# Kernel tuning notes

Measured on AMD Instinct MI355X. Metric: run time of the kernel, lower is better.

The kernel has to match this reference:

```python
import jax, jax.numpy as jnp
import numpy as np

COMMITMENT_COST = 0.25
NUM_EMBEDDINGS = 1024
EMBEDDING_DIM = 256


def setup_inputs() -> dict:
    key = jax.random.key(0)
    k1, k2 = jax.random.split(key)
    inputs = jax.random.normal(k1, (64, 256, 32, 32), dtype=jnp.float32)
    emb_w = jax.random.normal(k2, (NUM_EMBEDDINGS, EMBEDDING_DIM), dtype=jnp.float32)
    return {"inputs": inputs, "emb_w": emb_w}


def reference(inputs, emb_w):
    # NCHW -> NHWC, flatten to [N, D]
    x = jnp.transpose(inputs, (0, 2, 3, 1))  # [B, H, W, D]
    B, H, W, D = x.shape
    flat = x.reshape(-1, D)  # [N, D]

    distances = (
        jnp.sum(flat * flat, axis=1, keepdims=True)
        + jnp.sum(emb_w * emb_w, axis=1)
        - 2.0 * flat @ emb_w.T
    )
    idx = jnp.argmin(distances, axis=1)  # [N]

    # one-hot @ W is just a gather of codebook rows
    quantized = emb_w[idx].reshape(B, H, W, D)

    # avg_probs = mean of one-hot encodings = normalized codeword counts
    counts = jnp.zeros((NUM_EMBEDDINGS,), dtype=jnp.float32).at[idx].add(1.0)
    avg_probs = counts / flat.shape[0]
    perplexity = jnp.exp(-jnp.sum(avg_probs * jnp.log(avg_probs + 1e-10)))

    e_latent_loss = jnp.mean((jax.lax.stop_gradient(quantized) - x) ** 2)
    loss = COMMITMENT_COST * e_latent_loss

    # straight-through estimator
    quantized_st = x + jax.lax.stop_gradient(quantized - x)
    quantized_out = jnp.transpose(quantized_st, (0, 3, 1, 2))  # back to NCHW

    return loss, quantized_out, perplexity, idx.reshape(B, H, W)
```

## Files before the change

### kernel.cpp

```cpp
#include <hip/hip_runtime.h>
#include <hip/hip_bf16.h>
#include <math.h>

typedef _Float16 f16;
typedef __attribute__((ext_vector_type(8))) _Float16 f16x8;
typedef __attribute__((ext_vector_type(16))) float f32x16;

#define DIMS 256
#define NCODE 1024
#define NPTS 65536

#define OUT_Q_OFF 1
#define OUT_PERP_OFF 16777217
#define OUT_IDX_OFF 16777218

#define EHI_F32_OFF 4
#define ELO_F32_OFF (4 + 131072)

#define ESTRIDE 264
#define XSTRIDE 132

__global__ __launch_bounds__(256) void k_eprep(const float* __restrict__ ew,
                                               f16* __restrict__ ehi,
                                               f16* __restrict__ elo,
                                               float* __restrict__ enorm) {
    int w = threadIdx.x >> 6;
    int l = threadIdx.x & 63;
    int row = blockIdx.x * 4 + w;
    float4 v = *reinterpret_cast<const float4*>(ew + (size_t)row * DIMS + l * 4);
    float vv[4] = {v.x, v.y, v.z, v.w};
    __align__(8) f16 hh[4];
    __align__(8) f16 ll[4];
    float s = 0.0f;
    #pragma unroll
    for (int e = 0; e < 4; ++e) {
        f16 h = (f16)vv[e];
        hh[e] = h;
        ll[e] = (f16)(vv[e] - (float)h);
        s += vv[e] * vv[e];
    }
    *reinterpret_cast<float2*>(ehi + (size_t)row * DIMS + l * 4) = *reinterpret_cast<float2*>(hh);
    *reinterpret_cast<float2*>(elo + (size_t)row * DIMS + l * 4) = *reinterpret_cast<float2*>(ll);
    #pragma unroll
    for (int off = 32; off > 0; off >>= 1) s += __shfl_down(s, off);
    if (l == 0) enorm[row] = s;
}

__global__ __launch_bounds__(256, 2) void k_argmin_mfma(const float* __restrict__ x,
                                                        const f16* __restrict__ ehi,
                                                        const f16* __restrict__ elo,
                                                        const float* __restrict__ enorm,
                                                        int* __restrict__ out_idx) {
    __shared__ __align__(16) char smem[2 * 32 * ESTRIDE * 2];
    __shared__ float enorm_lds[NCODE];
    float* Xs = (float*)smem;
    f16* EHI = (f16*)smem;
    f16* ELO = (f16*)(smem + 32 * ESTRIDE * 2);

    const int t = threadIdx.x;
    const int wave = t >> 6;
    const int lane = t & 63;
    const int lrow = lane & 31;
    const int lhalf = lane >> 5;

    const int blk = blockIdx.x;
    const int b = blk >> 3;
    const int hw0 = (blk & 7) << 7;
    const float* xb = x + (size_t)b * (DIMS * 1024) + hw0;

    #pragma unroll
    for (int i = 0; i < 4; ++i) enorm_lds[t + 256 * i] = enorm[t + 256 * i];

    f16x8 ahi[16], alo[16];
    #pragma unroll
    for (int dc = 0; dc < 4; ++dc) {
        __syncthreads();
        #pragma unroll
        for (int i = 0; i < 8; ++i) {
            int d = (t >> 5) + 8 * i;
            int p4 = (t & 31) * 4;
            float4 v = *reinterpret_cast<const float4*>(xb + (size_t)(dc * 64 + d) * 1024 + p4);
            *reinterpret_cast<float4*>(&Xs[d * XSTRIDE + p4]) = v;
        }
        __syncthreads();
        int p = wave * 32 + lrow;
        #pragma unroll
        for (int kcl = 0; kcl < 4; ++kcl) {
            f16x8 h, l;
            #pragma unroll
            for (int e = 0; e < 8; ++e) {
                float xv = Xs[(kcl * 16 + lhalf * 8 + e) * XSTRIDE + p];
                f16 hi = (f16)xv;
                h[e] = hi;
                l[e] = (f16)(xv - (float)hi);
            }
            ahi[dc * 4 + kcl] = h;
            alo[dc * 4 + kcl] = l;
        }
    }

    float bestv[16];
    int besti[16];
    #pragma unroll
    for (int r = 0; r < 16; ++r) { bestv[r] = 3.4e38f; besti[r] = 0; }

    for (int rd = 0; rd < 32; ++rd) {
        const int code0 = rd * 32;
        __syncthreads();
        #pragma unroll
        for (int j = 0; j < 4; ++j) {
            int q = t + 256 * j;
            int row = q >> 5;
            int cc = q & 31;
            const f16* sh = ehi + (size_t)(code0 + row) * DIMS + cc * 8;
            const f16* sl = elo + (size_t)(code0 + row) * DIMS + cc * 8;
            float4 vh = *reinterpret_cast<const float4*>(sh);
            float4 vl = *reinterpret_cast<const float4*>(sl);
            *reinterpret_cast<float4*>((char*)EHI + row * (ESTRIDE * 2) + cc * 16) = vh;
            *reinterpret_cast<float4*>((char*)ELO + row * (ESTRIDE * 2) + cc * 16) = vl;
        }
        __syncthreads();

        f32x16 acc;
        #pragma unroll
        for (int r = 0; r < 16; ++r) acc[r] = 0.0f;

        #pragma unroll
        for (int kc = 0; kc < 16; ++kc) {
            f16x8 bh = *reinterpret_cast<const f16x8*>(
                (const char*)EHI + lrow * (ESTRIDE * 2) + (kc * 2 + lhalf) * 16);
            f16x8 bl = *reinterpret_cast<const f16x8*>(
                (const char*)ELO + lrow * (ESTRIDE * 2) + (kc * 2 + lhalf) * 16);
            acc = __builtin_amdgcn_mfma_f32_32x32x16_f16(ahi[kc], bh, acc, 0, 0, 0);
            acc = __builtin_amdgcn_mfma_f32_32x32x16_f16(ahi[kc], bl, acc, 0, 0, 0);
            acc = __builtin_amdgcn_mfma_f32_32x32x16_f16(alo[kc], bh, acc, 0, 0, 0);
        }

        float en = enorm_lds[code0 + lrow];
        int cw = code0 + lrow;
        #pragma unroll
        for (int r = 0; r < 16; ++r) {
            float s = fmaf(-2.0f, acc[r], en);
            if (s < bestv[r]) { bestv[r] = s; besti[r] = cw; }
        }
    }

    #pragma unroll
    for (int off = 1; off <= 16; off <<= 1) {
        #pragma unroll
        for (int r = 0; r < 16; ++r) {
            float ov = __shfl_xor(bestv[r], off);
            int oi = __shfl_xor(besti[r], off);
            if (ov < bestv[r] || (ov == bestv[r] && oi < besti[r])) {
                bestv[r] = ov;
                besti[r] = oi;
            }
        }
    }
    if (lrow == 0) {
        #pragma unroll
        for (int r = 0; r < 16; ++r) {
            int row = (r & 3) + 8 * (r >> 2) + 4 * lhalf;
            out_idx[blk * 128 + wave * 32 + row] = besti[r];
        }
    }
}

#define QSTRIDE 258
__global__ __launch_bounds__(512) void k_quant(const float* __restrict__ x,
                                               const float* __restrict__ ew,
                                               const int* __restrict__ idxv,
                                               float* __restrict__ out,
                                               float* __restrict__ loss_acc) {
    __shared__ float Eq[64 * QSTRIDE];
    __shared__ int ids[64];
    const int t = threadIdx.x;
    const int blk = blockIdx.x;
    const int b = blk >> 4;
    const int hw0 = (blk & 15) << 6;

    if (t < 64) ids[t] = idxv[(b << 10) + hw0 + t];
    __syncthreads();

    #pragma unroll
    for (int i = 0; i < 8; ++i) {
        int f = i * 512 + t;
        int row = f >> 6;
        int c4 = f & 63;
        float4 v = *reinterpret_cast<const float4*>(ew + (size_t)ids[row] * DIMS + c4 * 4);
        float2 lo2 = {v.x, v.y};
        float2 hi2 = {v.z, v.w};
        *reinterpret_cast<float2*>(&Eq[row * QSTRIDE + c4 * 4]) = lo2;
        *reinterpret_cast<float2*>(&Eq[row * QSTRIDE + c4 * 4 + 2]) = hi2;
    }
    __syncthreads();

    const int p = t & 63;
    const int c0 = t >> 6;
    float lsum = 0.0f;
    #pragma unroll
    for (int k = 0; k < 32; ++k) {
        int c = k * 8 + c0;
        unsigned g = ((unsigned)b << 18) | ((unsigned)c << 10) | (unsigned)(hw0 + p);
        float xv = x[g];
        float q = Eq[p * QSTRIDE + c];
        float d = q - xv;
        out[OUT_Q_OFF + g] = xv + d;
        lsum += d * d;
    }
    #pragma unroll
    for (int off = 32; off > 0; off >>= 1) lsum += __shfl_down(lsum, off);
    if ((t & 63) == 0) atomicAdd(&loss_acc[blk & 63], lsum);
}

__global__ __launch_bounds__(256) void k_hist(const int* __restrict__ idxv,
                                              int* __restrict__ counts,
                                              float* __restrict__ out) {
    __shared__ int h[NCODE];
    int t = threadIdx.x;
    #pragma unroll
    for (int i = 0; i < 4; ++i) h[t + 256 * i] = 0;
    __syncthreads();
    int base = blockIdx.x * 1024;
    #pragma unroll
    for (int i = 0; i < 4; ++i) {
        int n = base + t + 256 * i;
        int id = idxv[n];
        out[OUT_IDX_OFF + n] = (float)id;
        atomicAdd(&h[id], 1);
    }
    __syncthreads();
    #pragma unroll
    for (int i = 0; i < 4; ++i) {
        int v = h[t + 256 * i];
        if (v) atomicAdd(&counts[t + 256 * i], v);
    }
}

__global__ __launch_bounds__(256) void k_final(const int* __restrict__ counts,
                                               const float* __restrict__ loss_acc,
                                               float* __restrict__ out) {
    int t = threadIdx.x;
    float s = 0.0f;
    #pragma unroll
    for (int i = 0; i < 4; ++i) {
        int cnt = counts[t + 256 * i];
        float p = (float)cnt * (1.0f / 65536.0f);
        s += p * logf(p + 1e-10f);
    }
    #pragma unroll
    for (int off = 32; off > 0; off >>= 1) s += __shfl_down(s, off);
    __shared__ float wsum[4];
    if ((t & 63) == 0) wsum[t >> 6] = s;
    __syncthreads();
    if (t == 0) {
        float S = wsum[0] + wsum[1] + wsum[2] + wsum[3];
        out[OUT_PERP_OFF] = expf(-S);
        float ls = 0.0f;
        for (int i = 0; i < 64; ++i) ls += loss_acc[i];
        out[0] = 0.25f * (ls * (1.0f / 16777216.0f));
    }
}

extern "C" void kernel_launch(void* const* d_in, const int* in_sizes, int n_in,
                              void* d_out, int out_size, void* d_ws, size_t ws_size,
                              hipStream_t stream) {
    const float* x = (const float*)d_in[0];
    const float* ew = (const float*)d_in[1];
    float* out = (float*)d_out;
    float* ws = (float*)d_ws;

    float* loss_acc = ws;
    int* counts = (int*)(ws + 64);
    float* enorm = ws + 64 + 1024;
    int* idxv = (int*)(ws + 64 + 2048);

    f16* ehi = (f16*)(out + EHI_F32_OFF);
    f16* elo = (f16*)(out + ELO_F32_OFF);

    hipMemsetAsync(d_ws, 0, (64 + 1024) * sizeof(float), stream);

    k_eprep<<<256, 256, 0, stream>>>(ew, ehi, elo, enorm);
    k_argmin_mfma<<<512, 256, 0, stream>>>(x, ehi, elo, enorm, idxv);
    k_quant<<<1024, 512, 0, stream>>>(x, ew, idxv, out, loss_acc);
    k_hist<<<64, 256, 0, stream>>>(idxv, counts, out);
    k_final<<<1, 256, 0, stream>>>(counts, loss_acc, out);
}
```

Measured before the change: 200.4 us.

## Double-buffer codebook tiles via direct global-to-LDS loads with XOR-swizzled layout

The codebook prep kernel now writes the hi/lo fp16 planes in a pre-tiled, XOR-swizzled 32-row tile layout. The argmin kernel streams each tile straight into LDS with global_load_lds, double-buffered so the next tile's load overlaps the current tile's MFMA work. This removes the register round-trip and one of the two barriers per round, and the swizzle replaces padding to avoid LDS bank conflicts. LDS use grows to 64KB plus the norms, which may limit how many blocks fit per CU.

```diff
diff --git a/kernel.cpp b/kernel.cpp
--- a/kernel.cpp
+++ b/kernel.cpp
@@ -16,13 +16,19 @@
 
 #define EHI_F32_OFF 4
 #define ELO_F32_OFF (4 + 131072)
-
-#define ESTRIDE 264
+#define TILE_BYTES 16384
+
 #define XSTRIDE 132
 
+__device__ __forceinline__ void gload_lds16(const void* g, void* l) {
+    __builtin_amdgcn_global_load_lds(
+        (const __attribute__((address_space(1))) unsigned int*)g,
+        (__attribute__((address_space(3))) unsigned int*)l, 16, 0, 0);
+}
+
 __global__ __launch_bounds__(256) void k_eprep(const float* __restrict__ ew,
-                                               f16* __restrict__ ehi,
-                                               f16* __restrict__ elo,
+                                               char* __restrict__ ehi,
+                                               char* __restrict__ elo,
                                                float* __restrict__ enorm) {
     int w = threadIdx.x >> 6;
     int l = threadIdx.x & 63;
@@ -39,23 +45,23 @@
         ll[e] = (f16)(vv[e] - (float)h);
         s += vv[e] * vv[e];
     }
-    *reinterpret_cast<float2*>(ehi + (size_t)row * DIMS + l * 4) = *reinterpret_cast<float2*>(hh);
-    *reinterpret_cast<float2*>(elo + (size_t)row * DIMS + l * 4) = *reinterpret_cast<float2*>(ll);
-    #pragma unroll
-    for (int off = 32; off > 0; off >>= 1) s += __shfl_down(s, off);
+    size_t off = (size_t)(row >> 5) * TILE_BYTES + (size_t)(row & 31) * 512
+               + (size_t)((((l >> 1) ^ (row & 7)) << 4) + ((l & 1) << 3));
+    *reinterpret_cast<float2*>(ehi + off) = *reinterpret_cast<float2*>(hh);
+    *reinterpret_cast<float2*>(elo + off) = *reinterpret_cast<float2*>(ll);
+    #pragma unroll
+    for (int off2 = 32; off2 > 0; off2 >>= 1) s += __shfl_down(s, off2);
     if (l == 0) enorm[row] = s;
 }
 
 __global__ __launch_bounds__(256, 2) void k_argmin_mfma(const float* __restrict__ x,
-                                                        const f16* __restrict__ ehi,
-                                                        const f16* __restrict__ elo,
+                                                        const char* __restrict__ ehi,
+                                                        const char* __restrict__ elo,
                                                         const float* __restrict__ enorm,
                                                         int* __restrict__ out_idx) {
-    __shared__ __align__(16) char smem[2 * 32 * ESTRIDE * 2];
+    __shared__ __align__(16) char smem[2 * 2 * TILE_BYTES];
     __shared__ float enorm_lds[NCODE];
     float* Xs = (float*)smem;
-    f16* EHI = (f16*)smem;
-    f16* ELO = (f16*)(smem + 32 * ESTRIDE * 2);
 
     const int t = threadIdx.x;
     const int wave = t >> 6;
@@ -98,44 +104,54 @@
             alo[dc * 4 + kcl] = l;
         }
     }
+    __syncthreads();
+
+    const char* gplane = (wave >> 1) ? elo : ehi;
+    const int pl_off = (wave >> 1) * TILE_BYTES;
+    const int woff = (wave & 1) * 8192;
+
+    #pragma unroll
+    for (int i = 0; i < 8; ++i) {
+        int off = woff + i * 1024;
+        gload_lds16(gplane + off + lane * 16, smem + pl_off + off);
+    }
+    __syncthreads();
 
     float bestv[16];
     int besti[16];
     #pragma unroll
     for (int r = 0; r < 16; ++r) { bestv[r] = 3.4e38f; besti[r] = 0; }
 
+    int cur = 0;
     for (int rd = 0; rd < 32; ++rd) {
-        const int code0 = rd * 32;
-        __syncthreads();
-        #pragma unroll
-        for (int j = 0; j < 4; ++j) {
-            int q = t + 256 * j;
-            int row = q >> 5;
-            int cc = q & 31;
-            const f16* sh = ehi + (size_t)(code0 + row) * DIMS + cc * 8;
-            const f16* sl = elo + (size_t)(code0 + row) * DIMS + cc * 8;
-            float4 vh = *reinterpret_cast<const float4*>(sh);
-            float4 vl = *reinterpret_cast<const float4*>(sl);
-            *reinterpret_cast<float4*>((char*)EHI + row * (ESTRIDE * 2) + cc * 16) = vh;
-            *reinterpret_cast<float4*>((char*)ELO + row * (ESTRIDE * 2) + cc * 16) = vl;
-        }
-        __syncthreads();
-
+        if (rd + 1 < 32) {
+            const char* gp = gplane + (size_t)(rd + 1) * TILE_BYTES;
+            char* lp = smem + (cur ^ 1) * (2 * TILE_BYTES) + pl_off;
+            #pragma unroll
+            for (int i = 0; i < 8; ++i) {
+                int off = woff + i * 1024;
+                gload_lds16(gp + off + lane * 16, lp + off);
+            }
+        }
+
+        const char* EHb = smem + cur * (2 * TILE_BYTES);
+        const char* ELb = EHb + TILE_BYTES;
         f32x16 acc;
         #pragma unroll
         for (int r = 0; r < 16; ++r) acc[r] = 0.0f;
 
         #pragma unroll
         for (int kc = 0; kc < 16; ++kc) {
-            f16x8 bh = *reinterpret_cast<const f16x8*>(
-                (const char*)EHI + lrow * (ESTRIDE * 2) + (kc * 2 + lhalf) * 16);
-            f16x8 bl = *reinterpret_cast<const f16x8*>(
-                (const char*)ELO + lrow * (ESTRIDE * 2) + (kc * 2 + lhalf) * 16);
+            int g = kc * 2 + lhalf;
+            int ra = lrow * 512 + ((g ^ (lrow & 7)) << 4);
+            f16x8 bh = *reinterpret_cast<const f16x8*>(EHb + ra);
+            f16x8 bl = *reinterpret_cast<const f16x8*>(ELb + ra);
             acc = __builtin_amdgcn_mfma_f32_32x32x16_f16(ahi[kc], bh, acc, 0, 0, 0);
             acc = __builtin_amdgcn_mfma_f32_32x32x16_f16(ahi[kc], bl, acc, 0, 0, 0);
             acc = __builtin_amdgcn_mfma_f32_32x32x16_f16(alo[kc], bh, acc, 0, 0, 0);
         }
 
+        const int code0 = rd * 32;
         float en = enorm_lds[code0 + lrow];
         int cw = code0 + lrow;
         #pragma unroll
@@ -143,6 +159,9 @@
             float s = fmaf(-2.0f, acc[r], en);
             if (s < bestv[r]) { bestv[r] = s; besti[r] = cw; }
         }
+
+        __syncthreads();
+        cur ^= 1;
     }
 
     #pragma unroll
@@ -275,8 +294,8 @@
     float* enorm = ws + 64 + 1024;
     int* idxv = (int*)(ws + 64 + 2048);
 
-    f16* ehi = (f16*)(out + EHI_F32_OFF);
-    f16* elo = (f16*)(out + ELO_F32_OFF);
+    char* ehi = (char*)(out + EHI_F32_OFF);
+    char* elo = (char*)(out + ELO_F32_OFF);
 
     hipMemsetAsync(d_ws, 0, (64 + 1024) * sizeof(float), stream);
 
```

Measured after the change: 178.4 us. 11.0% less time.
